# Kernel optimization log

Measured on AMD Instinct MI355X. Metric: run time of the kernel, lower is better.

## Reference

```python
import jax, jax.numpy as jnp
import numpy as np

B, Lq, Lk, E = 4, 512, 512, 128
D = 2 * E  # input feature dim = 2*encode_size


def setup_inputs() -> dict:
    key = jax.random.key(0)
    ks = jax.random.split(key, 6)
    return {
        "query": jax.random.normal(ks[0], (B, Lq, D), jnp.float32),
        "key": jax.random.normal(ks[1], (B, Lk, D), jnp.float32),
        "value": jax.random.normal(ks[2], (B, Lq, D), jnp.float32),
        "Wc1": jax.random.normal(ks[3], (D, E), jnp.float32) / np.sqrt(D),
        "Wc2": jax.random.normal(ks[4], (D, E), jnp.float32) / np.sqrt(D),
        "vc": jax.random.normal(ks[5], (E,), jnp.float32) / np.sqrt(E),
    }


def reference(query, key, value, Wc1, Wc2, vc):
    # q: [B, Lq, E], k: [B, Lk, E]
    q = query @ Wc1
    k = key @ Wc2
    # additive (Bahdanau) scores: tanh(q + k) reduced by vc -> [B, Lk, Lq]
    sjt = jnp.einsum('blqe,e->blq', jnp.tanh(q[:, None, :, :] + k[:, :, None, :]), vc)
    atten = jax.nn.softmax(sjt, axis=2)  # softmax over Lq (dim=2), dropout p=0.0 is identity
    context = jnp.einsum('blq,bqd->bld', atten, value)  # [B, Lk, D]
    return (context, atten)
```

## Files before the change

### kernel.cpp

```cpp
#include <hip/hip_runtime.h>

#define NB 4
#define LQ 512
#define LK 512
#define EE 128
#define DD 256

__device__ __forceinline__ float fast_rcp(float x) { return __builtin_amdgcn_rcpf(x); }

__global__ __launch_bounds__(256) void proj_exp_kernel(
    const float* __restrict__ query, const float* __restrict__ key,
    const float* __restrict__ Wc1, const float* __restrict__ Wc2,
    float* __restrict__ EqT, float* __restrict__ Ek)
{
    __shared__ float in_s[8][DD];
    const int r0 = blockIdx.x * 8;
    const bool is_q = (r0 < NB * LQ);
    const float* src = is_q ? query : key;
    const float* W   = is_q ? Wc1   : Wc2;
    const int rbase  = is_q ? r0    : r0 - NB * LQ;

    const float4* srow4 = (const float4*)(src + (size_t)rbase * DD);
    #pragma unroll
    for (int i = 0; i < 2; ++i)
        ((float4*)in_s)[i * 256 + threadIdx.x] = srow4[i * 256 + threadIdx.x];
    __syncthreads();

    const int c  = threadIdx.x & 127;
    const int rg = threadIdx.x >> 7;
    float acc[4] = {0.f, 0.f, 0.f, 0.f};
    for (int d = 0; d < DD; d += 4) {
        const float w0 = W[(d + 0) * EE + c];
        const float w1 = W[(d + 1) * EE + c];
        const float w2 = W[(d + 2) * EE + c];
        const float w3 = W[(d + 3) * EE + c];
        #pragma unroll
        for (int i = 0; i < 4; ++i) {
            const float4 x = *(const float4*)&in_s[rg * 4 + i][d];
            acc[i] += x.x * w0 + x.y * w1 + x.z * w2 + x.w * w3;
        }
    }
    if (is_q) {
        const int b    = rbase >> 9;
        const int qloc = (rbase & 511) + rg * 4;
        float4 o;
        o.x = __expf(2.0f * acc[0]); o.y = __expf(2.0f * acc[1]);
        o.z = __expf(2.0f * acc[2]); o.w = __expf(2.0f * acc[3]);
        *(float4*)&EqT[((size_t)(b * EE + c)) * LQ + qloc] = o;
    } else {
        #pragma unroll
        for (int i = 0; i < 4; ++i)
            Ek[(size_t)(rbase + rg * 4 + i) * EE + c] = __expf(2.0f * acc[i]);
    }
}

__global__ __launch_bounds__(512) void atten_kernel(
    const float* __restrict__ EqT, const float* __restrict__ Ek,
    const float* __restrict__ vc, float* __restrict__ attn)
{
    __shared__ float  sj_s[4][LQ];
    __shared__ float2 mZ_s[4][2];
    __shared__ float  scale_s[4][2];
    const int b   = blockIdx.x >> 7;
    const int lt  = blockIdx.x & 127;
    const int l0  = lt * 4;
    const int tid = threadIdx.x;
    const int q   = tid;
    const float* eqc = EqT + (size_t)b * EE * LQ + q;
    const float* ekb = Ek  + ((size_t)b * LK + l0) * EE;

    float vcsum = 0.f;
    for (int e = 0; e < EE; e += 4) {
        const float4 v = *(const float4*)(vc + e);
        vcsum += (v.x + v.y) + (v.z + v.w);
    }

    float s2[4] = {0.f, 0.f, 0.f, 0.f};
    for (int e = 0; e < EE; e += 4) {
        const float a0 = eqc[(size_t)(e + 0) * LQ];
        const float a1 = eqc[(size_t)(e + 1) * LQ];
        const float a2 = eqc[(size_t)(e + 2) * LQ];
        const float a3 = eqc[(size_t)(e + 3) * LQ];
        const float4 vv = *(const float4*)(vc + e);
        #pragma unroll
        for (int l = 0; l < 4; ++l) {
            const float4 kk = *(const float4*)(ekb + l * EE + e);
            s2[l] += vv.x * fast_rcp(a0 * kk.x + 1.0f);
            s2[l] += vv.y * fast_rcp(a1 * kk.y + 1.0f);
            s2[l] += vv.z * fast_rcp(a2 * kk.z + 1.0f);
            s2[l] += vv.w * fast_rcp(a3 * kk.w + 1.0f);
        }
    }
    #pragma unroll
    for (int l = 0; l < 4; ++l)
        sj_s[l][q] = vcsum - 2.0f * s2[l];
    __syncthreads();

    const int w = tid >> 6, lane = tid & 63;
    const int l = w & 3, h2 = w >> 2, base = h2 * 256;
    float m = -1e30f;
    #pragma unroll
    for (int i = 0; i < 4; ++i) m = fmaxf(m, sj_s[l][base + lane + 64 * i]);
    #pragma unroll
    for (int off = 32; off >= 1; off >>= 1) m = fmaxf(m, __shfl_xor(m, off));
    float Z = 0.f;
    #pragma unroll
    for (int i = 0; i < 4; ++i) {
        const int idx = base + lane + 64 * i;
        const float ex = __expf(sj_s[l][idx] - m);
        sj_s[l][idx] = ex;
        Z += ex;
    }
    #pragma unroll
    for (int off = 32; off >= 1; off >>= 1) Z += __shfl_xor(Z, off);
    if (lane == 0) mZ_s[l][h2] = make_float2(m, Z);
    __syncthreads();
    if (lane == 0) {
        const float2 A = mZ_s[l][0], B2 = mZ_s[l][1];
        const float M  = fmaxf(A.x, B2.x);
        const float Zt = A.y * __expf(A.x - M) + B2.y * __expf(B2.x - M);
        scale_s[l][h2] = __expf((h2 ? B2.x : A.x) - M) * fast_rcp(Zt);
    }
    __syncthreads();

    #pragma unroll
    for (int li = 0; li < 4; ++li)
        attn[(size_t)(b * LK + l0 + li) * LQ + q] = sj_s[li][q] * scale_s[li][q >> 8];
}

__global__ __launch_bounds__(512) void context_kernel(
    const float* __restrict__ attn, const float* __restrict__ value,
    float* __restrict__ ctx)
{
    const int b    = blockIdx.x >> 6;
    const int lt   = blockIdx.x & 63;
    const int row0 = b * LK + lt * 8;
    const int tid  = threadIdx.x;
    const int g    = tid >> 6;
    const int lane = tid & 63;
    const float4* v4 = (const float4*)(value + (size_t)b * LQ * DD);

    float4 ac[8];
    #pragma unroll
    for (int l = 0; l < 8; ++l) ac[l] = make_float4(0.f, 0.f, 0.f, 0.f);

    const int q0 = g * 64;
    for (int q = q0; q < q0 + 64; q += 4) {
        float4 a[8];
        #pragma unroll
        for (int l = 0; l < 8; ++l)
            a[l] = *(const float4*)(attn + (size_t)(row0 + l) * LQ + q);
        const float4 v0 = v4[(size_t)(q + 0) * 64 + lane];
        const float4 v1 = v4[(size_t)(q + 1) * 64 + lane];
        const float4 v2 = v4[(size_t)(q + 2) * 64 + lane];
        const float4 v3 = v4[(size_t)(q + 3) * 64 + lane];
        #pragma unroll
        for (int l = 0; l < 8; ++l) {
            ac[l].x += a[l].x * v0.x; ac[l].y += a[l].x * v0.y;
            ac[l].z += a[l].x * v0.z; ac[l].w += a[l].x * v0.w;
            ac[l].x += a[l].y * v1.x; ac[l].y += a[l].y * v1.y;
            ac[l].z += a[l].y * v1.z; ac[l].w += a[l].y * v1.w;
            ac[l].x += a[l].z * v2.x; ac[l].y += a[l].z * v2.y;
            ac[l].z += a[l].z * v2.z; ac[l].w += a[l].z * v2.w;
            ac[l].x += a[l].w * v3.x; ac[l].y += a[l].w * v3.y;
            ac[l].z += a[l].w * v3.z; ac[l].w += a[l].w * v3.w;
        }
    }

    __shared__ float4 red[4][8][64];
    if (g >= 4) {
        #pragma unroll
        for (int l = 0; l < 8; ++l) red[g - 4][l][lane] = ac[l];
    }
    __syncthreads();
    if (g < 4) {
        #pragma unroll
        for (int l = 0; l < 8; ++l) {
            const float4 r = red[g][l][lane];
            ac[l].x += r.x; ac[l].y += r.y; ac[l].z += r.z; ac[l].w += r.w;
        }
    }
    __syncthreads();
    if (g == 2 || g == 3) {
        #pragma unroll
        for (int l = 0; l < 8; ++l) red[g - 2][l][lane] = ac[l];
    }
    __syncthreads();
    if (g < 2) {
        #pragma unroll
        for (int l = 0; l < 8; ++l) {
            const float4 r = red[g][l][lane];
            ac[l].x += r.x; ac[l].y += r.y; ac[l].z += r.z; ac[l].w += r.w;
        }
    }
    __syncthreads();
    if (g == 1) {
        #pragma unroll
        for (int l = 0; l < 8; ++l) red[0][l][lane] = ac[l];
    }
    __syncthreads();
    if (g == 0) {
        #pragma unroll
        for (int l = 0; l < 8; ++l) {
            const float4 r = red[0][l][lane];
            ac[l].x += r.x; ac[l].y += r.y; ac[l].z += r.z; ac[l].w += r.w;
            ((float4*)ctx)[(size_t)(row0 + l) * 64 + lane] = ac[l];
        }
    }
}

extern "C" void kernel_launch(void* const* d_in, const int* in_sizes, int n_in,
                              void* d_out, int out_size, void* d_ws, size_t ws_size,
                              hipStream_t stream) {
    const float* query = (const float*)d_in[0];
    const float* key   = (const float*)d_in[1];
    const float* value = (const float*)d_in[2];
    const float* Wc1   = (const float*)d_in[3];
    const float* Wc2   = (const float*)d_in[4];
    const float* vc    = (const float*)d_in[5];

    float* ctx  = (float*)d_out;
    float* attn = (float*)d_out + (size_t)NB * LK * DD;

    float* EqT = ctx;
    float* Ek  = ctx + (size_t)NB * LQ * EE;

    proj_exp_kernel<<<dim3(512), dim3(256), 0, stream>>>(query, key, Wc1, Wc2, EqT, Ek);
    atten_kernel<<<dim3(NB * (LK / 4)), dim3(512), 0, stream>>>(EqT, Ek, vc, attn);
    context_kernel<<<dim3(NB * (LK / 8)), dim3(512), 0, stream>>>(attn, value, ctx);
}
```

Before: 124.7 us.

## Halve rows per block in projection and context kernels, stage Ek/vc in LDS

The projection kernel now handles 4 rows per block instead of 8 and launches 1024 blocks, with the inner loop unrolled over 8 input features. The attention kernel stages its 4 key rows of exp(2k) and the vc vector in shared memory instead of reading them from global memory in the inner loop. The context kernel computes 4 output rows per block instead of 8 and launches twice as many blocks. The aim is more blocks to fill the GPU's compute units and cheaper repeated operand reads, at the cost of reloading the weights and the value matrix more times overall.

```diff
diff --git a/kernel.cpp b/kernel.cpp
--- a/kernel.cpp
+++ b/kernel.cpp
@@ -13,44 +13,47 @@
     const float* __restrict__ Wc1, const float* __restrict__ Wc2,
     float* __restrict__ EqT, float* __restrict__ Ek)
 {
-    __shared__ float in_s[8][DD];
-    const int r0 = blockIdx.x * 8;
+    __shared__ float in_s[4][DD];
+    const int r0 = blockIdx.x * 4;
     const bool is_q = (r0 < NB * LQ);
     const float* src = is_q ? query : key;
     const float* W   = is_q ? Wc1   : Wc2;
     const int rbase  = is_q ? r0    : r0 - NB * LQ;
 
-    const float4* srow4 = (const float4*)(src + (size_t)rbase * DD);
-    #pragma unroll
-    for (int i = 0; i < 2; ++i)
-        ((float4*)in_s)[i * 256 + threadIdx.x] = srow4[i * 256 + threadIdx.x];
+    ((float4*)in_s)[threadIdx.x] = ((const float4*)(src + (size_t)rbase * DD))[threadIdx.x];
     __syncthreads();
 
     const int c  = threadIdx.x & 127;
     const int rg = threadIdx.x >> 7;
-    float acc[4] = {0.f, 0.f, 0.f, 0.f};
-    for (int d = 0; d < DD; d += 4) {
-        const float w0 = W[(d + 0) * EE + c];
-        const float w1 = W[(d + 1) * EE + c];
-        const float w2 = W[(d + 2) * EE + c];
-        const float w3 = W[(d + 3) * EE + c];
-        #pragma unroll
-        for (int i = 0; i < 4; ++i) {
-            const float4 x = *(const float4*)&in_s[rg * 4 + i][d];
-            acc[i] += x.x * w0 + x.y * w1 + x.z * w2 + x.w * w3;
-        }
+    float acc0 = 0.f, acc1 = 0.f;
+    for (int d = 0; d < DD; d += 8) {
+        float w0 = W[(d + 0) * EE + c];
+        float w1 = W[(d + 1) * EE + c];
+        float w2 = W[(d + 2) * EE + c];
+        float w3 = W[(d + 3) * EE + c];
+        float w4 = W[(d + 4) * EE + c];
+        float w5 = W[(d + 5) * EE + c];
+        float w6 = W[(d + 6) * EE + c];
+        float w7 = W[(d + 7) * EE + c];
+        const float4 xa0 = *(const float4*)&in_s[rg * 2 + 0][d];
+        const float4 xb0 = *(const float4*)&in_s[rg * 2 + 0][d + 4];
+        const float4 xa1 = *(const float4*)&in_s[rg * 2 + 1][d];
+        const float4 xb1 = *(const float4*)&in_s[rg * 2 + 1][d + 4];
+        acc0 += xa0.x * w0 + xa0.y * w1 + xa0.z * w2 + xa0.w * w3
+              + xb0.x * w4 + xb0.y * w5 + xb0.z * w6 + xb0.w * w7;
+        acc1 += xa1.x * w0 + xa1.y * w1 + xa1.z * w2 + xa1.w * w3
+              + xb1.x * w4 + xb1.y * w5 + xb1.z * w6 + xb1.w * w7;
     }
     if (is_q) {
         const int b    = rbase >> 9;
-        const int qloc = (rbase & 511) + rg * 4;
-        float4 o;
-        o.x = __expf(2.0f * acc[0]); o.y = __expf(2.0f * acc[1]);
-        o.z = __expf(2.0f * acc[2]); o.w = __expf(2.0f * acc[3]);
-        *(float4*)&EqT[((size_t)(b * EE + c)) * LQ + qloc] = o;
+        const int qloc = (rbase & 511) + rg * 2;
+        float2 o;
+        o.x = __expf(2.0f * acc0);
+        o.y = __expf(2.0f * acc1);
+        *(float2*)&EqT[((size_t)(b * EE + c)) * LQ + qloc] = o;
     } else {
-        #pragma unroll
-        for (int i = 0; i < 4; ++i)
-            Ek[(size_t)(rbase + rg * 4 + i) * EE + c] = __expf(2.0f * acc[i]);
+        Ek[(size_t)(rbase + rg * 2 + 0) * EE + c] = __expf(2.0f * acc0);
+        Ek[(size_t)(rbase + rg * 2 + 1) * EE + c] = __expf(2.0f * acc1);
     }
 }
 
@@ -59,6 +62,8 @@
     const float* __restrict__ vc, float* __restrict__ attn)
 {
     __shared__ float  sj_s[4][LQ];
+    __shared__ float  ek_s[4][EE];
+    __shared__ float  vc_s[EE];
     __shared__ float2 mZ_s[4][2];
     __shared__ float  scale_s[4][2];
     const int b   = blockIdx.x >> 7;
@@ -69,9 +74,14 @@
     const float* eqc = EqT + (size_t)b * EE * LQ + q;
     const float* ekb = Ek  + ((size_t)b * LK + l0) * EE;
 
+    ((float*)ek_s)[tid] = ekb[tid];
+    if (tid < EE) vc_s[tid] = vc[tid];
+    __syncthreads();
+
     float vcsum = 0.f;
+    #pragma unroll
     for (int e = 0; e < EE; e += 4) {
-        const float4 v = *(const float4*)(vc + e);
+        const float4 v = *(const float4*)&vc_s[e];
         vcsum += (v.x + v.y) + (v.z + v.w);
     }
 
@@ -81,10 +91,10 @@
         const float a1 = eqc[(size_t)(e + 1) * LQ];
         const float a2 = eqc[(size_t)(e + 2) * LQ];
         const float a3 = eqc[(size_t)(e + 3) * LQ];
-        const float4 vv = *(const float4*)(vc + e);
-        #pragma unroll
-        for (int l = 0; l < 4; ++l) {
-            const float4 kk = *(const float4*)(ekb + l * EE + e);
+        const float4 vv = *(const float4*)&vc_s[e];
+        #pragma unroll
+        for (int l = 0; l < 4; ++l) {
+            const float4 kk = *(const float4*)&ek_s[l][e];
             s2[l] += vv.x * fast_rcp(a0 * kk.x + 1.0f);
             s2[l] += vv.y * fast_rcp(a1 * kk.y + 1.0f);
             s2[l] += vv.z * fast_rcp(a2 * kk.z + 1.0f);
@@ -132,30 +142,30 @@
     const float* __restrict__ attn, const float* __restrict__ value,
     float* __restrict__ ctx)
 {
-    const int b    = blockIdx.x >> 6;
-    const int lt   = blockIdx.x & 63;
-    const int row0 = b * LK + lt * 8;
+    const int b    = blockIdx.x >> 7;
+    const int lt   = blockIdx.x & 127;
+    const int row0 = b * LK + lt * 4;
     const int tid  = threadIdx.x;
     const int g    = tid >> 6;
     const int lane = tid & 63;
     const float4* v4 = (const float4*)(value + (size_t)b * LQ * DD);
 
-    float4 ac[8];
-    #pragma unroll
-    for (int l = 0; l < 8; ++l) ac[l] = make_float4(0.f, 0.f, 0.f, 0.f);
+    float4 ac[4];
+    #pragma unroll
+    for (int l = 0; l < 4; ++l) ac[l] = make_float4(0.f, 0.f, 0.f, 0.f);
 
     const int q0 = g * 64;
     for (int q = q0; q < q0 + 64; q += 4) {
-        float4 a[8];
-        #pragma unroll
-        for (int l = 0; l < 8; ++l)
+        float4 a[4];
+        #pragma unroll
+        for (int l = 0; l < 4; ++l)
             a[l] = *(const float4*)(attn + (size_t)(row0 + l) * LQ + q);
         const float4 v0 = v4[(size_t)(q + 0) * 64 + lane];
         const float4 v1 = v4[(size_t)(q + 1) * 64 + lane];
         const float4 v2 = v4[(size_t)(q + 2) * 64 + lane];
         const float4 v3 = v4[(size_t)(q + 3) * 64 + lane];
         #pragma unroll
-        for (int l = 0; l < 8; ++l) {
+        for (int l = 0; l < 4; ++l) {
             ac[l].x += a[l].x * v0.x; ac[l].y += a[l].x * v0.y;
             ac[l].z += a[l].x * v0.z; ac[l].w += a[l].x * v0.w;
             ac[l].x += a[l].y * v1.x; ac[l].y += a[l].y * v1.y;
@@ -167,15 +177,15 @@
         }
     }
 
-    __shared__ float4 red[4][8][64];
+    __shared__ float4 red[4][4][64];
     if (g >= 4) {
         #pragma unroll
-        for (int l = 0; l < 8; ++l) red[g - 4][l][lane] = ac[l];
+        for (int l = 0; l < 4; ++l) red[g - 4][l][lane] = ac[l];
     }
     __syncthreads();
     if (g < 4) {
         #pragma unroll
-        for (int l = 0; l < 8; ++l) {
+        for (int l = 0; l < 4; ++l) {
             const float4 r = red[g][l][lane];
             ac[l].x += r.x; ac[l].y += r.y; ac[l].z += r.z; ac[l].w += r.w;
         }
@@ -183,12 +193,12 @@
     __syncthreads();
     if (g == 2 || g == 3) {
         #pragma unroll
-        for (int l = 0; l < 8; ++l) red[g - 2][l][lane] = ac[l];
+        for (int l = 0; l < 4; ++l) red[g - 2][l][lane] = ac[l];
     }
     __syncthreads();
     if (g < 2) {
         #pragma unroll
-        for (int l = 0; l < 8; ++l) {
+        for (int l = 0; l < 4; ++l) {
             const float4 r = red[g][l][lane];
             ac[l].x += r.x; ac[l].y += r.y; ac[l].z += r.z; ac[l].w += r.w;
         }
@@ -196,12 +206,12 @@
     __syncthreads();
     if (g == 1) {
         #pragma unroll
-        for (int l = 0; l < 8; ++l) red[0][l][lane] = ac[l];
+        for (int l = 0; l < 4; ++l) red[0][l][lane] = ac[l];
     }
     __syncthreads();
     if (g == 0) {
         #pragma unroll
-        for (int l = 0; l < 8; ++l) {
+        for (int l = 0; l < 4; ++l) {
             const float4 r = red[0][l][lane];
             ac[l].x += r.x; ac[l].y += r.y; ac[l].z += r.z; ac[l].w += r.w;
             ((float4*)ctx)[(size_t)(row0 + l) * 64 + lane] = ac[l];
@@ -225,7 +235,7 @@
     float* EqT = ctx;
     float* Ek  = ctx + (size_t)NB * LQ * EE;
 
-    proj_exp_kernel<<<dim3(512), dim3(256), 0, stream>>>(query, key, Wc1, Wc2, EqT, Ek);
+    proj_exp_kernel<<<dim3(1024), dim3(256), 0, stream>>>(query, key, Wc1, Wc2, EqT, Ek);
     atten_kernel<<<dim3(NB * (LK / 4)), dim3(512), 0, stream>>>(EqT, Ek, vc, attn);
-    context_kernel<<<dim3(NB * (LK / 8)), dim3(512), 0, stream>>>(attn, value, ctx);
-}
+    context_kernel<<<dim3(NB * (LK / 4)), dim3(512), 0, stream>>>(attn, value, ctx);
+}
```

Result: slower. 128.3 us (+2.9%).

## Split attention E-reduction across thread groups and shrink context tiles

Applied to the files above, without the earlier changes.

The attention kernel now stages the key-exp rows and vc in shared memory. Each thread handles four query columns over a quarter of the E dimension, loading EqT as float4, and the partial sums are reduced through shared memory. This cuts redundant global loads of Ek and vc and widens the loads, at the cost of an extra shared-memory reduction step and more LDS use. The projection kernel's inner loop is unrolled by 8, and the context kernel processes 4 rows per block instead of 8, doubling the grid for better occupancy while reloading value more often.

```diff
diff --git a/kernel.cpp b/kernel.cpp
--- a/kernel.cpp
+++ b/kernel.cpp
@@ -29,15 +29,21 @@
     const int c  = threadIdx.x & 127;
     const int rg = threadIdx.x >> 7;
     float acc[4] = {0.f, 0.f, 0.f, 0.f};
-    for (int d = 0; d < DD; d += 4) {
+    for (int d = 0; d < DD; d += 8) {
         const float w0 = W[(d + 0) * EE + c];
         const float w1 = W[(d + 1) * EE + c];
         const float w2 = W[(d + 2) * EE + c];
         const float w3 = W[(d + 3) * EE + c];
+        const float w4 = W[(d + 4) * EE + c];
+        const float w5 = W[(d + 5) * EE + c];
+        const float w6 = W[(d + 6) * EE + c];
+        const float w7 = W[(d + 7) * EE + c];
         #pragma unroll
         for (int i = 0; i < 4; ++i) {
-            const float4 x = *(const float4*)&in_s[rg * 4 + i][d];
-            acc[i] += x.x * w0 + x.y * w1 + x.z * w2 + x.w * w3;
+            const float4 xa = *(const float4*)&in_s[rg * 4 + i][d];
+            const float4 xb = *(const float4*)&in_s[rg * 4 + i][d + 4];
+            acc[i] += xa.x * w0 + xa.y * w1 + xa.z * w2 + xa.w * w3
+                    + xb.x * w4 + xb.y * w5 + xb.z * w6 + xb.w * w7;
         }
     }
     if (is_q) {
@@ -58,6 +64,9 @@
     const float* __restrict__ EqT, const float* __restrict__ Ek,
     const float* __restrict__ vc, float* __restrict__ attn)
 {
+    __shared__ float  ek_s[4][EE];
+    __shared__ float  vc_s[EE];
+    __shared__ float  s2p_s[3][4][LQ];
     __shared__ float  sj_s[4][LQ];
     __shared__ float2 mZ_s[4][2];
     __shared__ float  scale_s[4][2];
@@ -65,35 +74,61 @@
     const int lt  = blockIdx.x & 127;
     const int l0  = lt * 4;
     const int tid = threadIdx.x;
-    const int q   = tid;
-    const float* eqc = EqT + (size_t)b * EE * LQ + q;
-    const float* ekb = Ek  + ((size_t)b * LK + l0) * EE;
+    const int qq  = tid & 127;
+    const int eg  = tid >> 7;
+
+    ((float*)ek_s)[tid] = Ek[((size_t)b * LK + l0) * EE + tid];
+    if (tid < EE) vc_s[tid] = vc[tid];
+    __syncthreads();
 
     float vcsum = 0.f;
+    #pragma unroll
     for (int e = 0; e < EE; e += 4) {
-        const float4 v = *(const float4*)(vc + e);
+        const float4 v = *(const float4*)&vc_s[e];
         vcsum += (v.x + v.y) + (v.z + v.w);
     }
 
-    float s2[4] = {0.f, 0.f, 0.f, 0.f};
-    for (int e = 0; e < EE; e += 4) {
-        const float a0 = eqc[(size_t)(e + 0) * LQ];
-        const float a1 = eqc[(size_t)(e + 1) * LQ];
-        const float a2 = eqc[(size_t)(e + 2) * LQ];
-        const float a3 = eqc[(size_t)(e + 3) * LQ];
-        const float4 vv = *(const float4*)(vc + e);
-        #pragma unroll
-        for (int l = 0; l < 4; ++l) {
-            const float4 kk = *(const float4*)(ekb + l * EE + e);
-            s2[l] += vv.x * fast_rcp(a0 * kk.x + 1.0f);
-            s2[l] += vv.y * fast_rcp(a1 * kk.y + 1.0f);
-            s2[l] += vv.z * fast_rcp(a2 * kk.z + 1.0f);
-            s2[l] += vv.w * fast_rcp(a3 * kk.w + 1.0f);
-        }
-    }
-    #pragma unroll
-    for (int l = 0; l < 4; ++l)
-        sj_s[l][q] = vcsum - 2.0f * s2[l];
+    const float4* eq4 = (const float4*)(EqT + (size_t)b * EE * LQ);
+    float s2[4][4];
+    #pragma unroll
+    for (int l = 0; l < 4; ++l) { s2[l][0]=0.f; s2[l][1]=0.f; s2[l][2]=0.f; s2[l][3]=0.f; }
+
+    #pragma unroll 4
+    for (int i = 0; i < 32; ++i) {
+        const int e = eg * 32 + i;
+        const float4 a  = eq4[(size_t)e * 128 + qq];
+        const float  vv = vc_s[e];
+        #pragma unroll
+        for (int l = 0; l < 4; ++l) {
+            const float kk = ek_s[l][e];
+            s2[l][0] += vv * fast_rcp(a.x * kk + 1.0f);
+            s2[l][1] += vv * fast_rcp(a.y * kk + 1.0f);
+            s2[l][2] += vv * fast_rcp(a.z * kk + 1.0f);
+            s2[l][3] += vv * fast_rcp(a.w * kk + 1.0f);
+        }
+    }
+
+    if (eg > 0) {
+        #pragma unroll
+        for (int l = 0; l < 4; ++l)
+            *(float4*)&s2p_s[eg - 1][l][qq * 4] =
+                make_float4(s2[l][0], s2[l][1], s2[l][2], s2[l][3]);
+    }
+    __syncthreads();
+    if (eg == 0) {
+        #pragma unroll
+        for (int l = 0; l < 4; ++l) {
+            const float4 p0 = *(const float4*)&s2p_s[0][l][qq * 4];
+            const float4 p1 = *(const float4*)&s2p_s[1][l][qq * 4];
+            const float4 p2 = *(const float4*)&s2p_s[2][l][qq * 4];
+            float4 sj;
+            sj.x = vcsum - 2.0f * (s2[l][0] + p0.x + p1.x + p2.x);
+            sj.y = vcsum - 2.0f * (s2[l][1] + p0.y + p1.y + p2.y);
+            sj.z = vcsum - 2.0f * (s2[l][2] + p0.z + p1.z + p2.z);
+            sj.w = vcsum - 2.0f * (s2[l][3] + p0.w + p1.w + p2.w);
+            *(float4*)&sj_s[l][qq * 4] = sj;
+        }
+    }
     __syncthreads();
 
     const int w = tid >> 6, lane = tid & 63;
@@ -123,6 +158,7 @@
     }
     __syncthreads();
 
+    const int q = tid;
     #pragma unroll
     for (int li = 0; li < 4; ++li)
         attn[(size_t)(b * LK + l0 + li) * LQ + q] = sj_s[li][q] * scale_s[li][q >> 8];
@@ -132,30 +168,30 @@
     const float* __restrict__ attn, const float* __restrict__ value,
     float* __restrict__ ctx)
 {
-    const int b    = blockIdx.x >> 6;
-    const int lt   = blockIdx.x & 63;
-    const int row0 = b * LK + lt * 8;
+    const int b    = blockIdx.x >> 7;
+    const int lt   = blockIdx.x & 127;
+    const int row0 = b * LK + lt * 4;
     const int tid  = threadIdx.x;
     const int g    = tid >> 6;
     const int lane = tid & 63;
     const float4* v4 = (const float4*)(value + (size_t)b * LQ * DD);
 
-    float4 ac[8];
-    #pragma unroll
-    for (int l = 0; l < 8; ++l) ac[l] = make_float4(0.f, 0.f, 0.f, 0.f);
+    float4 ac[4];
+    #pragma unroll
+    for (int l = 0; l < 4; ++l) ac[l] = make_float4(0.f, 0.f, 0.f, 0.f);
 
     const int q0 = g * 64;
     for (int q = q0; q < q0 + 64; q += 4) {
-        float4 a[8];
-        #pragma unroll
-        for (int l = 0; l < 8; ++l)
+        float4 a[4];
+        #pragma unroll
+        for (int l = 0; l < 4; ++l)
             a[l] = *(const float4*)(attn + (size_t)(row0 + l) * LQ + q);
         const float4 v0 = v4[(size_t)(q + 0) * 64 + lane];
         const float4 v1 = v4[(size_t)(q + 1) * 64 + lane];
         const float4 v2 = v4[(size_t)(q + 2) * 64 + lane];
         const float4 v3 = v4[(size_t)(q + 3) * 64 + lane];
         #pragma unroll
-        for (int l = 0; l < 8; ++l) {
+        for (int l = 0; l < 4; ++l) {
             ac[l].x += a[l].x * v0.x; ac[l].y += a[l].x * v0.y;
             ac[l].z += a[l].x * v0.z; ac[l].w += a[l].x * v0.w;
             ac[l].x += a[l].y * v1.x; ac[l].y += a[l].y * v1.y;
@@ -167,15 +203,15 @@
         }
     }
 
-    __shared__ float4 red[4][8][64];
+    __shared__ float4 red[4][4][64];
     if (g >= 4) {
         #pragma unroll
-        for (int l = 0; l < 8; ++l) red[g - 4][l][lane] = ac[l];
+        for (int l = 0; l < 4; ++l) red[g - 4][l][lane] = ac[l];
     }
     __syncthreads();
     if (g < 4) {
         #pragma unroll
-        for (int l = 0; l < 8; ++l) {
+        for (int l = 0; l < 4; ++l) {
             const float4 r = red[g][l][lane];
             ac[l].x += r.x; ac[l].y += r.y; ac[l].z += r.z; ac[l].w += r.w;
         }
@@ -183,12 +219,12 @@
     __syncthreads();
     if (g == 2 || g == 3) {
         #pragma unroll
-        for (int l = 0; l < 8; ++l) red[g - 2][l][lane] = ac[l];
+        for (int l = 0; l < 4; ++l) red[g - 2][l][lane] = ac[l];
     }
     __syncthreads();
     if (g < 2) {
         #pragma unroll
-        for (int l = 0; l < 8; ++l) {
+        for (int l = 0; l < 4; ++l) {
             const float4 r = red[g][l][lane];
             ac[l].x += r.x; ac[l].y += r.y; ac[l].z += r.z; ac[l].w += r.w;
         }
@@ -196,12 +232,12 @@
     __syncthreads();
     if (g == 1) {
         #pragma unroll
-        for (int l = 0; l < 8; ++l) red[0][l][lane] = ac[l];
+        for (int l = 0; l < 4; ++l) red[0][l][lane] = ac[l];
     }
     __syncthreads();
     if (g == 0) {
         #pragma unroll
-        for (int l = 0; l < 8; ++l) {
+        for (int l = 0; l < 4; ++l) {
             const float4 r = red[0][l][lane];
             ac[l].x += r.x; ac[l].y += r.y; ac[l].z += r.z; ac[l].w += r.w;
             ((float4*)ctx)[(size_t)(row0 + l) * 64 + lane] = ac[l];
@@ -227,5 +263,5 @@
 
     proj_exp_kernel<<<dim3(512), dim3(256), 0, stream>>>(query, key, Wc1, Wc2, EqT, Ek);
     atten_kernel<<<dim3(NB * (LK / 4)), dim3(512), 0, stream>>>(EqT, Ek, vc, attn);
-    context_kernel<<<dim3(NB * (LK / 8)), dim3(512), 0, stream>>>(attn, value, ctx);
-}
+    context_kernel<<<dim3(NB * (LK / 4)), dim3(512), 0, stream>>>(attn, value, ctx);
+}
```

Measured after the change: 121.3 us. -2.7%, faster.
